# Performance work log

Hardware: AMD Instinct MI355X
Metric: run time of the kernel (lower is better)

## Reference

```python
import jax, jax.numpy as jnp
import numpy as np

B, N, C, H, CLS = 16, 1024, 768, 12, 1000
M = 0.5  # amax init for alpha


def setup_inputs() -> dict:
    key = jax.random.key(0)
    k = jax.random.split(key, 7)
    x = jax.random.normal(k[0], (B, N, C), jnp.float32)
    label = jax.random.randint(k[1], (B,), 0, CLS)
    # alpha is initialized to ones*m in the module; add small noise so gating is non-trivial
    alpha = jnp.ones((CLS, 3 * C), jnp.float32) * M + 0.1 * jax.random.normal(k[2], (CLS, 3 * C), jnp.float32)
    qkv_w = jax.random.normal(k[3], (3 * C, C), jnp.float32) * 0.02
    qkv_b = jax.random.normal(k[4], (3 * C,), jnp.float32) * 0.02
    proj_w = jax.random.normal(k[5], (C, C), jnp.float32) * 0.02
    proj_b = jax.random.normal(k[6], (C,), jnp.float32) * 0.02
    return {"x": x, "label": label, "alpha": alpha, "qkv_w": qkv_w,
            "qkv_b": qkv_b, "proj_w": proj_w, "proj_b": proj_b}


def reference(x, label, alpha, qkv_w, qkv_b, proj_w, proj_b):
    b, n, c = x.shape
    h = H
    hd = c // h
    scale = hd ** -0.5
    # per-sample sigmoid gate over the 3C output rows of the qkv projection
    sig = jax.nn.sigmoid(alpha[label])  # (B, 3C)
    # F.linear(x_i, W * s_i[:,None], b * s_i) == (x_i @ W.T) * s_i + b * s_i
    qkv = jnp.einsum('bnc,dc->bnd', x, qkv_w) * sig[:, None, :] + (qkv_b * sig)[:, None, :]
    qkv = qkv.reshape(b, n, 3, h, hd).transpose(2, 0, 3, 1, 4)  # (3, B, H, N, hd)
    q, k_, v = qkv[0], qkv[1], qkv[2]
    attn = jax.nn.softmax(jnp.einsum('bhqd,bhkd->bhqk', q, k_) * scale, axis=-1)
    out = jnp.einsum('bhqk,bhkd->bhqd', attn, v)          # (B, H, N, hd)
    out = out.transpose(0, 2, 1, 3).reshape(b, n, c)       # (B, N, C)
    out = out @ proj_w.T + proj_b
    return out
```

## Files before the change

kernel.cpp:

```cpp
#include <hip/hip_runtime.h>

typedef __bf16 bf16;
typedef __attribute__((ext_vector_type(8))) __bf16 bf16x8;
typedef __attribute__((ext_vector_type(4))) float floatx4;
typedef __attribute__((ext_vector_type(8))) short short8;
typedef __attribute__((ext_vector_type(4))) short short4v;
typedef unsigned short u16;

#define B_  16
#define N_  1024
#define C_  768
#define H_  12
#define HD_ 64
#define TC_ 2304
#define QSZ (B_ * H_ * N_ * HD_)

__device__ __forceinline__ u16 f2b(float f) { bf16 h = (bf16)f; return __builtin_bit_cast(u16, h); }
__device__ __forceinline__ float b2f(u16 b) { return (float)__builtin_bit_cast(bf16, b); }

typedef __attribute__((address_space(1))) const unsigned int guint;
typedef __attribute__((address_space(3))) unsigned int luint;
__device__ __forceinline__ void gl16(const u16* g, u16* l) {
    __builtin_amdgcn_global_load_lds((guint*)g, (luint*)l, 16, 0, 0);
}

__device__ __forceinline__ short8 ld8(const void* p, int idx, int isf32) {
    if (isf32) {
        const float* f = (const float*)p + idx;
        floatx4 a = *(const floatx4*)f;
        floatx4 c = *(const floatx4*)(f + 4);
        short8 r;
        r[0] = (short)f2b(a[0]); r[1] = (short)f2b(a[1]);
        r[2] = (short)f2b(a[2]); r[3] = (short)f2b(a[3]);
        r[4] = (short)f2b(c[0]); r[5] = (short)f2b(c[1]);
        r[6] = (short)f2b(c[2]); r[7] = (short)f2b(c[3]);
        return r;
    }
    return *(const short8*)((const u16*)p + idx);
}
__device__ __forceinline__ float ldf(const void* p, int idx, int isf32) {
    return isf32 ? ((const float*)p)[idx] : b2f(((const u16*)p)[idx]);
}

__global__ void dtype_probe(const u16* __restrict__ x, int* __restrict__ flag) {
    __shared__ int cnt;
    if (threadIdx.x == 0) cnt = 0;
    __syncthreads();
    unsigned e = (x[threadIdx.x] >> 7) & 0xFF;
    atomicAdd(&cnt, (e >= 170 || e == 0) ? 1 : 0);
    __syncthreads();
    if (threadIdx.x == 0) flag[0] = (cnt >= 32) ? 1 : 0;
}

__global__ void swz_inplace(u16* __restrict__ x, u16* __restrict__ qw,
                            u16* __restrict__ pw, const int* __restrict__ dflag)
{
    if (dflag[0] != 0) return;
    const int gid = blockIdx.x * 256 + threadIdx.x;
    const int b   = gid & 7;
    const int rb  = gid >> 3;
    const int row = rb / 12, g = rb - row * 12;
    u16* base; int r;
    if (row < 16384)      { base = x;  r = row; }
    else if (row < 18688) { base = qw; r = row - 16384; }
    else                  { base = pw; r = row - 18688; }
    u16* rp = base + (size_t)r * 768 + g * 64;
    short8 v = *(const short8*)(rp + b * 8);
    *(short8*)(rp + (b ^ (r & 7)) * 8) = v;
}

template <int MODE, int F32>
__device__ __forceinline__ void gemm_body(
    const void* __restrict__ A, const void* __restrict__ W,
    const void* __restrict__ bias, const void* __restrict__ alpha,
    const int* __restrict__ label, void* __restrict__ out,
    u16* __restrict__ vT, const int* __restrict__ dflag)
{
    __shared__ __align__(16) u16 sm[16384];
    if ((dflag[0] != 0) != (F32 != 0)) return;
    u16* sA = sm;
    u16* sB = sm + 8192;
    const int t  = threadIdx.x;
    const int w  = t >> 6, l = t & 63;
    const int lr = l & 15, lq = l >> 4;
    const int id = blockIdx.x;
    const int xcd = id & 7, j = id >> 3;
    const int m0 = (xcd * 16 + (j & 15)) << 7;
    const int n0 = (j >> 4) << 7;
    const int wm = (w >> 1) << 6, wn = (w & 1) << 6;
    const int sw = lr & 7;

    floatx4 acc[4][4];
#pragma unroll
    for (int a = 0; a < 4; a++)
#pragma unroll
        for (int b = 0; b < 4; b++) acc[a][b] = (floatx4){0.f, 0.f, 0.f, 0.f};

    const int cx8  = (t & 7) * 8;
    const int row0 = t >> 3;

    auto a_off = [&](int r, int ks) -> int {
        const int m = m0 + r;
        if (MODE == 0) return m * 768 + ks * 64 + cx8;
        return (((m >> 10) * H_ + ks) * N_ + (m & (N_ - 1))) * HD_ + cx8;
    };

    auto compute = [&]() {
#pragma unroll
        for (int kc = 0; kc < 2; kc++) {
            bf16x8 af[4], bfr[4];
#pragma unroll
            for (int mt = 0; mt < 4; mt++)
                af[mt] = *(const bf16x8*)(sA + (wm + mt * 16 + lr) * 64 + 8 * ((kc * 4 + lq) ^ sw));
#pragma unroll
            for (int nt = 0; nt < 4; nt++)
                bfr[nt] = *(const bf16x8*)(sB + (wn + nt * 16 + lr) * 64 + 8 * ((kc * 4 + lq) ^ sw));
#pragma unroll
            for (int mt = 0; mt < 4; mt++)
#pragma unroll
                for (int nt = 0; nt < 4; nt++)
                    acc[mt][nt] = __builtin_amdgcn_mfma_f32_16x16x32_bf16(af[mt], bfr[nt], acc[mt][nt], 0, 0, 0);
        }
    };

    const int nk = 12;
    if (F32 == 0) {
        const u16* A16 = (const u16*)A;
        const u16* W16 = (const u16*)W;
        for (int ks = 0; ks < nk; ++ks) {
            __syncthreads();
#pragma unroll
            for (int i = 0; i < 4; i++) {
                gl16(A16 + a_off(row0 + 32 * i, ks), sA + i * 2048 + t * 8);
                gl16(W16 + (n0 + row0 + 32 * i) * 768 + ks * 64 + cx8, sB + i * 2048 + t * 8);
            }
            __syncthreads();
            compute();
        }
    } else {
        const int wblk = 8 * ((t & 7) ^ ((t >> 3) & 7));
        const int aoffw = (MODE == 0) ? wblk : (t & 7) * 8;
        short8 ra[4], rb[4];
#pragma unroll
        for (int i = 0; i < 4; i++) {
            ra[i] = ld8(A, a_off(row0 + 32 * i, 0), (MODE == 0) ? 1 : 0);
            rb[i] = ld8(W, (n0 + row0 + 32 * i) * 768 + cx8, 1);
        }
        for (int ks = 0; ks < nk; ++ks) {
            __syncthreads();
#pragma unroll
            for (int i = 0; i < 4; i++) {
                *(short8*)(sA + (row0 + 32 * i) * 64 + aoffw) = ra[i];
                *(short8*)(sB + (row0 + 32 * i) * 64 + wblk)  = rb[i];
            }
            __syncthreads();
            if (ks + 1 < nk) {
#pragma unroll
                for (int i = 0; i < 4; i++) {
                    ra[i] = ld8(A, a_off(row0 + 32 * i, ks + 1), (MODE == 0) ? 1 : 0);
                    rb[i] = ld8(W, (n0 + row0 + 32 * i) * 768 + (ks + 1) * 64 + cx8, 1);
                }
            }
            compute();
        }
    }

    if (MODE == 0) {
        const int b   = m0 >> 10;
        const int lab = label[b];
        const int which = (n0 >= 1536) ? 2 : (n0 >= 768 ? 1 : 0);
        if (which == 2) {
#pragma unroll
            for (int nt = 0; nt < 4; nt++) {
                const int d3   = n0 + wn + nt * 16 + lr;
                const float sg = 1.f / (1.f + __expf(-ldf(alpha, lab * TC_ + d3, F32)));
                const float bv = ldf(bias, d3, F32);
                const int rcol = d3 - 1536;
                const int h = rcol >> 6, dd = rcol & 63;
                u16* vp = vT + (((b * H_ + h) * HD_ + dd) << 10);
#pragma unroll
                for (int mt = 0; mt < 4; mt++) {
                    const int nb = (m0 & 1023) + wm + mt * 16 + lq * 4;
                    const int sidx = (nb & ~63) + 8 * (((nb >> 3) & 7) ^ (dd & 7)) + (nb & 7);
                    short4v pk;
#pragma unroll
                    for (int i = 0; i < 4; i++) pk[i] = (short)f2b((acc[mt][nt][i] + bv) * sg);
                    *(short4v*)(vp + sidx) = pk;
                }
            }
        } else {
            float sgv[4], bvv[4];
#pragma unroll
            for (int nt = 0; nt < 4; nt++) {
                const int d3 = n0 + wn + nt * 16 + lr;
                sgv[nt] = 1.f / (1.f + __expf(-ldf(alpha, lab * TC_ + d3, F32)));
                bvv[nt] = ldf(bias, d3, F32);
            }
            const int hbase = (n0 - which * 768) >> 6;
            const int nb0   = m0 & 1023;
            u16* ob = (u16*)out + which * QSZ;
#pragma unroll
            for (int p = 0; p < 2; p++) {
                __syncthreads();
                if (wm == p * 64) {
#pragma unroll
                    for (int nt = 0; nt < 4; nt++) {
                        const int c = wn + nt * 16 + lr;
#pragma unroll
                        for (int mt = 0; mt < 4; mt++)
#pragma unroll
                            for (int i = 0; i < 4; i++)
                                sm[(mt * 16 + lq * 4 + i) * 132 + c] =
                                    f2b((acc[mt][nt][i] + bvv[nt]) * sgv[nt]);
                    }
                }
                __syncthreads();
#pragma unroll
                for (int hh = 0; hh < 2; hh++) {
                    u16* dsth = ob + ((((b * H_ + hbase + hh) << 10) + nb0 + p * 64) << 6);
#pragma unroll
                    for (int mi = 0; mi < 2; mi++) {
                        const int m = (t >> 3) + 32 * mi;
                        *(short8*)(dsth + m * 64 + (t & 7) * 8) =
                            *(const short8*)(sm + m * 132 + hh * 64 + 8 * ((t & 7) ^ (m & 7)));
                    }
                }
            }
        }
    } else {
        if (F32) {
#pragma unroll
            for (int nt = 0; nt < 4; nt++) {
                const int n    = n0 + wn + nt * 16 + lr;
                const float bv = ldf(bias, n, 1);
#pragma unroll
                for (int mt = 0; mt < 4; mt++)
#pragma unroll
                    for (int i = 0; i < 4; i++) {
                        const int m = m0 + wm + mt * 16 + lq * 4 + i;
                        ((float*)out)[m * C_ + n] = acc[mt][nt][i] + bv;
                    }
            }
        } else {
#pragma unroll
            for (int p = 0; p < 2; p++) {
                __syncthreads();
                if (wm == p * 64) {
#pragma unroll
                    for (int nt = 0; nt < 4; nt++) {
                        const int c    = wn + nt * 16 + lr;
                        const float bv = ldf(bias, n0 + c, 0);
#pragma unroll
                        for (int mt = 0; mt < 4; mt++)
#pragma unroll
                            for (int i = 0; i < 4; i++)
                                sm[(mt * 16 + lq * 4 + i) * 132 + c] = f2b(acc[mt][nt][i] + bv);
                    }
                }
                __syncthreads();
                u16* o = (u16*)out;
#pragma unroll
                for (int mi = 0; mi < 4; mi++) {
                    const int mm = (t >> 4) + 16 * mi;
                    const int n8 = (t & 15) * 8;
                    *(short8*)(o + (m0 + p * 64 + mm) * C_ + n0 + n8) =
                        *(const short8*)(sm + mm * 132 + n8);
                }
            }
        }
    }
}

__global__ __launch_bounds__(256, 4) void gemm0_bf16(
    const void* A, const void* W, const void* bias, const void* alpha,
    const int* label, void* out, u16* vT, const int* dflag)
{ gemm_body<0, 0>(A, W, bias, alpha, label, out, vT, dflag); }

__global__ __launch_bounds__(256, 3) void gemm0_f32(
    const void* A, const void* W, const void* bias, const void* alpha,
    const int* label, void* out, u16* vT, const int* dflag)
{ gemm_body<0, 1>(A, W, bias, alpha, label, out, vT, dflag); }

__global__ __launch_bounds__(256, 4) void gemm1_bf16(
    const void* A, const void* W, const void* bias, const void* alpha,
    const int* label, void* out, u16* vT, const int* dflag)
{ gemm_body<1, 0>(A, W, bias, alpha, label, out, vT, dflag); }

__global__ __launch_bounds__(256, 3) void gemm1_f32(
    const void* A, const void* W, const void* bias, const void* alpha,
    const int* label, void* out, u16* vT, const int* dflag)
{ gemm_body<1, 1>(A, W, bias, alpha, label, out, vT, dflag); }

__global__ __launch_bounds__(256, 4) void attn_fwd(
    u16* __restrict__ qb, const u16* __restrict__ kb, const u16* __restrict__ vtb)
{
    __shared__ __align__(16) u16 sQP[64 * 64];
    __shared__ __align__(16) u16 sK[2][64 * 64];
    __shared__ __align__(16) u16 sVt[2][64 * 64];

    const int t = threadIdx.x, w = t >> 6, l = t & 63;
    const int lr = l & 15, lq = l >> 4;
    const int id = blockIdx.x;
    const int r8 = id & 7, s = id >> 3;
    const int bh = r8 * 24 + (s >> 4);
    const int q0 = (s & 15) << 6;
    const int sw = lr & 7;

    u16* qg = qb + (bh * N_ + q0) * HD_;
    gl16(qg + t * 8,        sQP + t * 8);
    gl16(qg + 2048 + t * 8, sQP + 2048 + t * 8);
    __syncthreads();
    bf16x8 qf[2];
#pragma unroll
    for (int kc = 0; kc < 2; kc++)
        qf[kc] = *(const bf16x8*)(sQP + (w * 16 + lr) * 64 + 8 * ((kc * 4 + lq) ^ sw));

    float l_run = 0.f;
    floatx4 o_acc[4];
#pragma unroll
    for (int nt = 0; nt < 4; nt++) o_acc[nt] = (floatx4){0.f, 0.f, 0.f, 0.f};

    const u16* kgb = kb + bh * (N_ * HD_);
    const u16* vgb = vtb + bh * (HD_ * N_);
    const int vrow = t >> 3, vcol = (t & 7) * 8;

    for (int kt2 = 0; kt2 < 8; ++kt2) {
        __syncthreads();
        const u16* gk = kgb + kt2 * 8192;
        gl16(gk + t * 8,        sK[0] + t * 8);
        gl16(gk + 2048 + t * 8, sK[0] + 2048 + t * 8);
        gl16(gk + 4096 + t * 8, sK[1] + t * 8);
        gl16(gk + 6144 + t * 8, sK[1] + 2048 + t * 8);
        const u16* gv = vgb + kt2 * 128;
        gl16(gv + vrow * N_ + vcol,             sVt[0] + t * 8);
        gl16(gv + (vrow + 32) * N_ + vcol,      sVt[0] + 2048 + t * 8);
        gl16(gv + vrow * N_ + 64 + vcol,        sVt[1] + t * 8);
        gl16(gv + (vrow + 32) * N_ + 64 + vcol, sVt[1] + 2048 + t * 8);
        __syncthreads();

#pragma unroll
        for (int hf = 0; hf < 2; hf++) {
            floatx4 st[4];
#pragma unroll
            for (int mt = 0; mt < 4; mt++) st[mt] = (floatx4){0.f, 0.f, 0.f, 0.f};
#pragma unroll
            for (int kc = 0; kc < 2; kc++) {
#pragma unroll
                for (int mt = 0; mt < 4; mt++) {
                    bf16x8 kf = *(const bf16x8*)(sK[hf] + (mt * 16 + lr) * 64 + 8 * ((kc * 4 + lq) ^ sw));
                    st[mt] = __builtin_amdgcn_mfma_f32_16x16x32_bf16(kf, qf[kc], st[mt], 0, 0, 0);
                }
            }
            float rs = 0.f;
            u16 pb[4][4];
#pragma unroll
            for (int mt = 0; mt < 4; mt++) {
#pragma unroll
                for (int i = 0; i < 4; i++) {
                    const float p = __expf(fmaf(st[mt][i], 0.125f, -8.0f));
                    pb[mt][i] = f2b(p);
                    rs += p;
                }
            }
            rs += __shfl_xor(rs, 16, 64);
            rs += __shfl_xor(rs, 32, 64);
            l_run += rs;
#pragma unroll
            for (int mt = 0; mt < 4; mt++) {
                short4v pk;
#pragma unroll
                for (int i = 0; i < 4; i++) pk[i] = (short)pb[mt][i];
                *(short4v*)(sQP + (w * 16 + lr) * 64 +
                            8 * ((mt * 2 + (lq >> 1)) ^ sw) + (lq & 1) * 4) = pk;
            }
#pragma unroll
            for (int kc = 0; kc < 2; kc++) {
                bf16x8 pf = *(const bf16x8*)(sQP + (w * 16 + lr) * 64 + 8 * ((kc * 4 + lq) ^ sw));
#pragma unroll
                for (int nt = 0; nt < 4; nt++) {
                    bf16x8 vf = *(const bf16x8*)(sVt[hf] + (nt * 16 + lr) * 64 + 8 * ((kc * 4 + lq) ^ sw));
                    o_acc[nt] = __builtin_amdgcn_mfma_f32_16x16x32_bf16(pf, vf, o_acc[nt], 0, 0, 0);
                }
            }
        }
    }

    const float linv = 1.f / l_run;
#pragma unroll
    for (int nt = 0; nt < 4; nt++) {
#pragma unroll
        for (int i = 0; i < 4; i++) {
            const float lv = __shfl(linv, lq * 4 + i, 64);
            const int row = w * 16 + lq * 4 + i;
            sQP[row * 64 + 8 * ((nt * 2 + (lr >> 3)) ^ (row & 7)) + (lr & 7)] = f2b(o_acc[nt][i] * lv);
        }
    }
    __syncthreads();
#pragma unroll
    for (int i2 = 0; i2 < 2; i2++) {
        const int idx = i2 * 2048 + t * 8;
        *(short8*)(qg + idx) = *(const short8*)(sQP + idx);
    }
}

extern "C" void kernel_launch(void* const* d_in, const int* in_sizes, int n_in,
                              void* d_out, int out_size, void* d_ws, size_t ws_size,
                              hipStream_t stream)
{
    void* x      = d_in[0];
    const int* label = (const int*)d_in[1];
    const void* alpha  = d_in[2];
    void* qkv_w  = d_in[3];
    const void* qkv_b  = d_in[4];
    void* proj_w = d_in[5];
    const void* proj_b = d_in[6];

    int* dflag = (int*)d_ws;
    u16* qbuf  = (u16*)((char*)d_ws + 256);
    u16* kbuf  = qbuf + QSZ;
    u16* vtbuf = kbuf + QSZ;

    dtype_probe<<<1, 512, 0, stream>>>((const u16*)x, dflag);
    swz_inplace<<<7296, 256, 0, stream>>>((u16*)x, (u16*)qkv_w, (u16*)proj_w, dflag);
    gemm0_bf16<<<2304, 256, 0, stream>>>(x, qkv_w, qkv_b, alpha, label, qbuf, vtbuf, dflag);
    gemm0_f32 <<<2304, 256, 0, stream>>>(x, qkv_w, qkv_b, alpha, label, qbuf, vtbuf, dflag);
    attn_fwd<<<3072, 256, 0, stream>>>(qbuf, kbuf, vtbuf);
    gemm1_bf16<<<768, 256, 0, stream>>>(qbuf, proj_w, proj_b, nullptr, nullptr, d_out, nullptr, dflag);
    gemm1_f32 <<<768, 256, 0, stream>>>(qbuf, proj_w, proj_b, nullptr, nullptr, d_out, nullptr, dflag);
}
```

Measured before the change: 346.4 us.

## Pre-convert fp32 inputs to swizzled bf16 and use direct-to-LDS GEMM loads

Removes the runtime dtype probe and the dual bf16/fp32 kernel variants. A single pass now converts fp32 x, qkv_w and proj_w into swizzled bf16 workspace copies. Both GEMMs can then always use the global_load_lds path with higher occupancy, instead of the fp32 register-staged path. The output projection writes fp32 through an LDS-staged, coalesced epilogue. In exchange there is an extra conversion pass that reads and writes about 60MB of activations.

```diff
diff --git a/kernel.cpp b/kernel.cpp
--- a/kernel.cpp
+++ b/kernel.cpp
@@ -16,7 +16,6 @@
 #define QSZ (B_ * H_ * N_ * HD_)
 
 __device__ __forceinline__ u16 f2b(float f) { bf16 h = (bf16)f; return __builtin_bit_cast(u16, h); }
-__device__ __forceinline__ float b2f(u16 b) { return (float)__builtin_bit_cast(bf16, b); }
 
 typedef __attribute__((address_space(1))) const unsigned int guint;
 typedef __attribute__((address_space(3))) unsigned int luint;
@@ -24,60 +23,37 @@
     __builtin_amdgcn_global_load_lds((guint*)g, (luint*)l, 16, 0, 0);
 }
 
-__device__ __forceinline__ short8 ld8(const void* p, int idx, int isf32) {
-    if (isf32) {
-        const float* f = (const float*)p + idx;
-        floatx4 a = *(const floatx4*)f;
-        floatx4 c = *(const floatx4*)(f + 4);
-        short8 r;
-        r[0] = (short)f2b(a[0]); r[1] = (short)f2b(a[1]);
-        r[2] = (short)f2b(a[2]); r[3] = (short)f2b(a[3]);
-        r[4] = (short)f2b(c[0]); r[5] = (short)f2b(c[1]);
-        r[6] = (short)f2b(c[2]); r[7] = (short)f2b(c[3]);
-        return r;
-    }
-    return *(const short8*)((const u16*)p + idx);
-}
-__device__ __forceinline__ float ldf(const void* p, int idx, int isf32) {
-    return isf32 ? ((const float*)p)[idx] : b2f(((const u16*)p)[idx]);
-}
-
-__global__ void dtype_probe(const u16* __restrict__ x, int* __restrict__ flag) {
-    __shared__ int cnt;
-    if (threadIdx.x == 0) cnt = 0;
-    __syncthreads();
-    unsigned e = (x[threadIdx.x] >> 7) & 0xFF;
-    atomicAdd(&cnt, (e >= 170 || e == 0) ? 1 : 0);
-    __syncthreads();
-    if (threadIdx.x == 0) flag[0] = (cnt >= 32) ? 1 : 0;
-}
-
-__global__ void swz_inplace(u16* __restrict__ x, u16* __restrict__ qw,
-                            u16* __restrict__ pw, const int* __restrict__ dflag)
+__global__ __launch_bounds__(256) void cvt_swz(
+    const float* __restrict__ x, const float* __restrict__ qw,
+    const float* __restrict__ pw, u16* __restrict__ xb,
+    u16* __restrict__ qwb, u16* __restrict__ pwb)
 {
-    if (dflag[0] != 0) return;
     const int gid = blockIdx.x * 256 + threadIdx.x;
     const int b   = gid & 7;
     const int rb  = gid >> 3;
     const int row = rb / 12, g = rb - row * 12;
-    u16* base; int r;
-    if (row < 16384)      { base = x;  r = row; }
-    else if (row < 18688) { base = qw; r = row - 16384; }
-    else                  { base = pw; r = row - 18688; }
-    u16* rp = base + (size_t)r * 768 + g * 64;
-    short8 v = *(const short8*)(rp + b * 8);
-    *(short8*)(rp + (b ^ (r & 7)) * 8) = v;
-}
-
-template <int MODE, int F32>
-__device__ __forceinline__ void gemm_body(
-    const void* __restrict__ A, const void* __restrict__ W,
-    const void* __restrict__ bias, const void* __restrict__ alpha,
-    const int* __restrict__ label, void* __restrict__ out,
-    u16* __restrict__ vT, const int* __restrict__ dflag)
+    const float* src; u16* dst; int r;
+    if (row < 16384)      { src = x;  dst = xb;  r = row; }
+    else if (row < 18688) { src = qw; dst = qwb; r = row - 16384; }
+    else                  { src = pw; dst = pwb; r = row - 18688; }
+    const float* sp = src + (size_t)r * 768 + g * 64 + b * 8;
+    floatx4 a = *(const floatx4*)sp;
+    floatx4 c = *(const floatx4*)(sp + 4);
+    short8 v;
+    v[0] = (short)f2b(a[0]); v[1] = (short)f2b(a[1]);
+    v[2] = (short)f2b(a[2]); v[3] = (short)f2b(a[3]);
+    v[4] = (short)f2b(c[0]); v[5] = (short)f2b(c[1]);
+    v[6] = (short)f2b(c[2]); v[7] = (short)f2b(c[3]);
+    *(short8*)(dst + (size_t)r * 768 + g * 64 + (b ^ (r & 7)) * 8) = v;
+}
+
+template <int MODE>
+__global__ __launch_bounds__(256, 4) void gemm_bt(
+    const u16* __restrict__ A, const u16* __restrict__ W,
+    const float* __restrict__ bias, const float* __restrict__ alpha,
+    const int* __restrict__ label, void* __restrict__ out, u16* __restrict__ vT)
 {
     __shared__ __align__(16) u16 sm[16384];
-    if ((dflag[0] != 0) != (F32 != 0)) return;
     u16* sA = sm;
     u16* sB = sm + 8192;
     const int t  = threadIdx.x;
@@ -105,7 +81,15 @@
         return (((m >> 10) * H_ + ks) * N_ + (m & (N_ - 1))) * HD_ + cx8;
     };
 
-    auto compute = [&]() {
+    const int nk = 12;
+    for (int ks = 0; ks < nk; ++ks) {
+        __syncthreads();
+#pragma unroll
+        for (int i = 0; i < 4; i++) {
+            gl16(A + a_off(row0 + 32 * i, ks), sA + i * 2048 + t * 8);
+            gl16(W + (n0 + row0 + 32 * i) * 768 + ks * 64 + cx8, sB + i * 2048 + t * 8);
+        }
+        __syncthreads();
 #pragma unroll
         for (int kc = 0; kc < 2; kc++) {
             bf16x8 af[4], bfr[4];
@@ -120,48 +104,6 @@
 #pragma unroll
                 for (int nt = 0; nt < 4; nt++)
                     acc[mt][nt] = __builtin_amdgcn_mfma_f32_16x16x32_bf16(af[mt], bfr[nt], acc[mt][nt], 0, 0, 0);
-        }
-    };
-
-    const int nk = 12;
-    if (F32 == 0) {
-        const u16* A16 = (const u16*)A;
-        const u16* W16 = (const u16*)W;
-        for (int ks = 0; ks < nk; ++ks) {
-            __syncthreads();
-#pragma unroll
-            for (int i = 0; i < 4; i++) {
-                gl16(A16 + a_off(row0 + 32 * i, ks), sA + i * 2048 + t * 8);
-                gl16(W16 + (n0 + row0 + 32 * i) * 768 + ks * 64 + cx8, sB + i * 2048 + t * 8);
-            }
-            __syncthreads();
-            compute();
-        }
-    } else {
-        const int wblk = 8 * ((t & 7) ^ ((t >> 3) & 7));
-        const int aoffw = (MODE == 0) ? wblk : (t & 7) * 8;
-        short8 ra[4], rb[4];
-#pragma unroll
-        for (int i = 0; i < 4; i++) {
-            ra[i] = ld8(A, a_off(row0 + 32 * i, 0), (MODE == 0) ? 1 : 0);
-            rb[i] = ld8(W, (n0 + row0 + 32 * i) * 768 + cx8, 1);
-        }
-        for (int ks = 0; ks < nk; ++ks) {
-            __syncthreads();
-#pragma unroll
-            for (int i = 0; i < 4; i++) {
-                *(short8*)(sA + (row0 + 32 * i) * 64 + aoffw) = ra[i];
-                *(short8*)(sB + (row0 + 32 * i) * 64 + wblk)  = rb[i];
-            }
-            __syncthreads();
-            if (ks + 1 < nk) {
-#pragma unroll
-                for (int i = 0; i < 4; i++) {
-                    ra[i] = ld8(A, a_off(row0 + 32 * i, ks + 1), (MODE == 0) ? 1 : 0);
-                    rb[i] = ld8(W, (n0 + row0 + 32 * i) * 768 + (ks + 1) * 64 + cx8, 1);
-                }
-            }
-            compute();
         }
     }
 
@@ -173,8 +115,8 @@
 #pragma unroll
             for (int nt = 0; nt < 4; nt++) {
                 const int d3   = n0 + wn + nt * 16 + lr;
-                const float sg = 1.f / (1.f + __expf(-ldf(alpha, lab * TC_ + d3, F32)));
-                const float bv = ldf(bias, d3, F32);
+                const float sg = 1.f / (1.f + __expf(-alpha[lab * TC_ + d3]));
+                const float bv = bias[d3];
                 const int rcol = d3 - 1536;
                 const int h = rcol >> 6, dd = rcol & 63;
                 u16* vp = vT + (((b * H_ + h) * HD_ + dd) << 10);
@@ -193,8 +135,8 @@
 #pragma unroll
             for (int nt = 0; nt < 4; nt++) {
                 const int d3 = n0 + wn + nt * 16 + lr;
-                sgv[nt] = 1.f / (1.f + __expf(-ldf(alpha, lab * TC_ + d3, F32)));
-                bvv[nt] = ldf(bias, d3, F32);
+                sgv[nt] = 1.f / (1.f + __expf(-alpha[lab * TC_ + d3]));
+                bvv[nt] = bias[d3];
             }
             const int hbase = (n0 - which * 768) >> 6;
             const int nb0   = m0 & 1023;
@@ -228,68 +170,26 @@
             }
         }
     } else {
-        if (F32) {
-#pragma unroll
-            for (int nt = 0; nt < 4; nt++) {
-                const int n    = n0 + wn + nt * 16 + lr;
-                const float bv = ldf(bias, n, 1);
-#pragma unroll
-                for (int mt = 0; mt < 4; mt++)
-#pragma unroll
-                    for (int i = 0; i < 4; i++) {
-                        const int m = m0 + wm + mt * 16 + lq * 4 + i;
-                        ((float*)out)[m * C_ + n] = acc[mt][nt][i] + bv;
-                    }
-            }
-        } else {
-#pragma unroll
-            for (int p = 0; p < 2; p++) {
-                __syncthreads();
-                if (wm == p * 64) {
-#pragma unroll
-                    for (int nt = 0; nt < 4; nt++) {
-                        const int c    = wn + nt * 16 + lr;
-                        const float bv = ldf(bias, n0 + c, 0);
-#pragma unroll
-                        for (int mt = 0; mt < 4; mt++)
-#pragma unroll
-                            for (int i = 0; i < 4; i++)
-                                sm[(mt * 16 + lq * 4 + i) * 132 + c] = f2b(acc[mt][nt][i] + bv);
-                    }
-                }
-                __syncthreads();
-                u16* o = (u16*)out;
-#pragma unroll
-                for (int mi = 0; mi < 4; mi++) {
-                    const int mm = (t >> 4) + 16 * mi;
-                    const int n8 = (t & 15) * 8;
-                    *(short8*)(o + (m0 + p * 64 + mm) * C_ + n0 + n8) =
-                        *(const short8*)(sm + mm * 132 + n8);
-                }
-            }
-        }
-    }
-}
-
-__global__ __launch_bounds__(256, 4) void gemm0_bf16(
-    const void* A, const void* W, const void* bias, const void* alpha,
-    const int* label, void* out, u16* vT, const int* dflag)
-{ gemm_body<0, 0>(A, W, bias, alpha, label, out, vT, dflag); }
-
-__global__ __launch_bounds__(256, 3) void gemm0_f32(
-    const void* A, const void* W, const void* bias, const void* alpha,
-    const int* label, void* out, u16* vT, const int* dflag)
-{ gemm_body<0, 1>(A, W, bias, alpha, label, out, vT, dflag); }
-
-__global__ __launch_bounds__(256, 4) void gemm1_bf16(
-    const void* A, const void* W, const void* bias, const void* alpha,
-    const int* label, void* out, u16* vT, const int* dflag)
-{ gemm_body<1, 0>(A, W, bias, alpha, label, out, vT, dflag); }
-
-__global__ __launch_bounds__(256, 3) void gemm1_f32(
-    const void* A, const void* W, const void* bias, const void* alpha,
-    const int* label, void* out, u16* vT, const int* dflag)
-{ gemm_body<1, 1>(A, W, bias, alpha, label, out, vT, dflag); }
+        float bvv[4];
+#pragma unroll
+        for (int nt = 0; nt < 4; nt++) bvv[nt] = bias[n0 + wn + nt * 16 + lr];
+        __syncthreads();
+        float* swf = (float*)sm + w * (16 * 68);
+        const int rr = l >> 2, c0 = (l & 3) * 16;
+#pragma unroll
+        for (int mt = 0; mt < 4; mt++) {
+#pragma unroll
+            for (int nt = 0; nt < 4; nt++)
+#pragma unroll
+                for (int i = 0; i < 4; i++)
+                    swf[(lq * 4 + i) * 68 + nt * 16 + lr] = acc[mt][nt][i] + bvv[nt];
+            float* drow = (float*)out + (m0 + wm + mt * 16 + rr) * 768 + n0 + wn + c0;
+#pragma unroll
+            for (int jj = 0; jj < 4; jj++)
+                *(floatx4*)(drow + jj * 4) = *(const floatx4*)(swf + rr * 68 + c0 + jj * 4);
+        }
+    }
+}
 
 __global__ __launch_bounds__(256, 4) void attn_fwd(
     u16* __restrict__ qb, const u16* __restrict__ kb, const u16* __restrict__ vtb)
@@ -407,24 +307,23 @@
                               void* d_out, int out_size, void* d_ws, size_t ws_size,
                               hipStream_t stream)
 {
-    void* x      = d_in[0];
-    const int* label = (const int*)d_in[1];
-    const void* alpha  = d_in[2];
-    void* qkv_w  = d_in[3];
-    const void* qkv_b  = d_in[4];
-    void* proj_w = d_in[5];
-    const void* proj_b = d_in[6];
-
-    int* dflag = (int*)d_ws;
-    u16* qbuf  = (u16*)((char*)d_ws + 256);
+    const float* x      = (const float*)d_in[0];
+    const int*   label  = (const int*)d_in[1];
+    const float* alpha  = (const float*)d_in[2];
+    const float* qkv_w  = (const float*)d_in[3];
+    const float* qkv_b  = (const float*)d_in[4];
+    const float* proj_w = (const float*)d_in[5];
+    const float* proj_b = (const float*)d_in[6];
+
+    u16* xb    = (u16*)d_ws;
+    u16* qwb   = xb + (size_t)16384 * 768;
+    u16* pwb   = qwb + (size_t)2304 * 768;
+    u16* qbuf  = pwb + (size_t)768 * 768;
     u16* kbuf  = qbuf + QSZ;
     u16* vtbuf = kbuf + QSZ;
 
-    dtype_probe<<<1, 512, 0, stream>>>((const u16*)x, dflag);
-    swz_inplace<<<7296, 256, 0, stream>>>((u16*)x, (u16*)qkv_w, (u16*)proj_w, dflag);
-    gemm0_bf16<<<2304, 256, 0, stream>>>(x, qkv_w, qkv_b, alpha, label, qbuf, vtbuf, dflag);
-    gemm0_f32 <<<2304, 256, 0, stream>>>(x, qkv_w, qkv_b, alpha, label, qbuf, vtbuf, dflag);
+    cvt_swz<<<7296, 256, 0, stream>>>(x, qkv_w, proj_w, xb, qwb, pwb);
+    gemm_bt<0><<<2304, 256, 0, stream>>>(xb, qwb, qkv_b, alpha, label, qbuf, vtbuf);
     attn_fwd<<<3072, 256, 0, stream>>>(qbuf, kbuf, vtbuf);
-    gemm1_bf16<<<768, 256, 0, stream>>>(qbuf, proj_w, proj_b, nullptr, nullptr, d_out, nullptr, dflag);
-    gemm1_f32 <<<768, 256, 0, stream>>>(qbuf, proj_w, proj_b, nullptr, nullptr, d_out, nullptr, dflag);
-}
+    gemm_bt<1><<<768, 256, 0, stream>>>(qbuf, pwb, proj_b, nullptr, nullptr, d_out, nullptr);
+}
```

After: 324.4 us. 6.3% less time.
